# Optimization experiments

Hardware: AMD Instinct MI355X
Metric: run time of the kernel (lower is better)

Reference implementation:

```python
import jax, jax.numpy as jnp
import numpy as np
import math

E = 500_000   # edges
N = 2_000     # nodes (small so duplicate (src,dst) pairs form real groups)
D = 128       # embedding_dim == n_heads*qkv_dim
H = 8         # heads
DK = 16       # qkv_dim
HH = 256      # hyper hidden
EMBD = 2      # hyper embd_dim
CLIP = 10.0   # tanh_clipping


def setup_inputs() -> dict:
    key = jax.random.key(0)
    ks = jax.random.split(key, 12)
    # shared_nodes: inverse indices of unique edge (src,dst) columns (reset() preprocessing)
    rng = np.random.default_rng(0)
    edge_indices = rng.integers(0, N, size=(2, E))
    _, inv = np.unique(edge_indices, axis=1, return_inverse=True)
    shared_nodes = jnp.asarray(inv.reshape(-1), dtype=jnp.int32)

    def lin(k, shape, fan_in):
        return jax.random.normal(k, shape, jnp.float32) / np.sqrt(fan_in)

    return {
        "pref": jax.random.uniform(ks[0], (2,), jnp.float32),
        "dists": jax.random.uniform(ks[1], (E, 2), jnp.float32),
        "edge_emb": jax.random.normal(ks[2], (E, D), jnp.float32),
        "shared_nodes": shared_nodes,
        "fc1_w": lin(ks[3], (HH, 2), 2), "fc1_b": jnp.zeros((HH,), jnp.float32),
        "fc2_w": lin(ks[4], (HH, HH), HH), "fc2_b": jnp.zeros((HH,), jnp.float32),
        "fc3_w": lin(ks[5], (2 * EMBD, HH), HH), "fc3_b": jnp.zeros((2 * EMBD,), jnp.float32),
        "wq_w": lin(ks[6], (D * H * DK, EMBD), EMBD),
        "wk_w": lin(ks[7], (D * H * DK, EMBD), EMBD),
    }


def reference(pref, dists, edge_emb, shared_nodes,
              fc1_w, fc1_b, fc2_w, fc2_b, fc3_w, fc3_b, wq_w, wk_w):
    # --- assign(pref): hypernetwork producing Wq, Wk (no activations, per source) ---
    h = pref @ fc1_w.T + fc1_b
    h = h @ fc2_w.T + fc2_b
    mid = h @ fc3_w.T + fc3_b                    # [4]
    Wq = (mid[:EMBD] @ wq_w.T).reshape(D, H * DK)
    Wk = (mid[EMBD:2 * EMBD] @ wk_w.T).reshape(D, H * DK)

    # --- reset(): scalarized distances + group means over shared edge groups ---
    d = pref[0] * dists[:, 0] + pref[1] * dists[:, 1]   # [E]
    n_edges = edge_emb.shape[0]
    seg = shared_nodes
    group_sums = jax.ops.segment_sum(edge_emb, seg, num_segments=n_edges)
    counts = jax.ops.segment_sum(jnp.ones((n_edges,), edge_emb.dtype), seg,
                                 num_segments=n_edges)
    group_means = group_sums / jnp.clip(counts, 1.0)[:, None]
    q = group_means[seg]                          # [E, D]

    # --- forward(): edge-wise multi-head dot score, tanh clip, group softmax ---
    fq = (q @ Wq.T).reshape(n_edges, H, DK)       # F.linear(q, Wq) (D == H*DK)
    fk = (edge_emb @ Wk.T).reshape(n_edges, H, DK)
    score = (fq * fk).sum(-1).mean(-1) / math.sqrt(D) - d / math.sqrt(2.0)
    score = CLIP * jnp.tanh(score)

    seg_max = jax.ops.segment_max(score, seg, num_segments=n_edges)
    ex = jnp.exp(score - seg_max[seg])
    denom = jax.ops.segment_sum(ex, seg, num_segments=n_edges)
    probs = ex / denom[seg]
    return probs[:, None]                         # [E, 1]
```

## Files before the change

kernel.cpp:

```cpp
#include <hip/hip_runtime.h>
#include <math.h>

#define DD 128
#define HHID 256
#define SLOTS 8


__global__ void k_setup(const float* __restrict__ pref,
                        const float* __restrict__ fc1_w, const float* __restrict__ fc1_b,
                        const float* __restrict__ fc2_w, const float* __restrict__ fc2_b,
                        const float* __restrict__ fc3_w, const float* __restrict__ fc3_b,
                        const float* __restrict__ wq_w, const float* __restrict__ wk_w,
                        const int* __restrict__ seg, unsigned* __restrict__ cs,
                        int* __restrict__ mem, float* __restrict__ M_, int E_) {
    if (blockIdx.x >= 64) {
        int base = ((int)(blockIdx.x - 64) * blockDim.x + threadIdx.x) * 4;
        if (base + 3 < E_) {
            int4 s4 = *(const int4*)&seg[base];
            unsigned j0 = atomicAdd(&cs[s4.x], 1u);
            unsigned j1 = atomicAdd(&cs[s4.y], 1u);
            unsigned j2 = atomicAdd(&cs[s4.z], 1u);
            unsigned j3 = atomicAdd(&cs[s4.w], 1u);
            if (j0 < SLOTS) mem[(size_t)s4.x * SLOTS + j0] = base + 0;
            if (j1 < SLOTS) mem[(size_t)s4.y * SLOTS + j1] = base + 1;
            if (j2 < SLOTS) mem[(size_t)s4.z * SLOTS + j2] = base + 2;
            if (j3 < SLOTS) mem[(size_t)s4.w * SLOTS + j3] = base + 3;
        } else {
            for (int e = base; e < E_; ++e) {
                int g = seg[e];
                unsigned j = atomicAdd(&cs[g], 1u);
                if (j < SLOTS) mem[(size_t)g * SLOTS + j] = e;
            }
        }
        return;
    }
    __shared__ float h1[HHID];
    __shared__ float h2[HHID];
    __shared__ float mid[4];
    __shared__ float wqv[2 * DD];
    int t = threadIdx.x;
    float p0 = pref[0], p1 = pref[1];
    h1[t] = fc1_w[t * 2 + 0] * p0 + fc1_w[t * 2 + 1] * p1 + fc1_b[t];
    __syncthreads();
    float acc = fc2_b[t];
    for (int i = 0; i < HHID; ++i) acc += fc2_w[t * HHID + i] * h1[i];
    h2[t] = acc;
    __syncthreads();
    if (t < 4) {
        float m = fc3_b[t];
        for (int i = 0; i < HHID; ++i) m += fc3_w[t * HHID + i] * h2[i];
        mid[t] = m;
    }
    __syncthreads();
    float m0 = mid[0], m1 = mid[1], m2 = mid[2], m3 = mid[3];
    {
        int a = t & 127, rh = t >> 7;
        int r = blockIdx.x * 2 + rh;
        wqv[rh * DD + a] = wq_w[(a * DD + r) * 2 + 0] * m0 + wq_w[(a * DD + r) * 2 + 1] * m1;
    }
    __syncthreads();
    int rh = t >> 7;
    int r = blockIdx.x * 2 + rh;
    int c = t & 127;
    const float scale = 0.011048543456f;
    float s = 0.f;
    for (int a = 0; a < DD; ++a) {
        float wk = wk_w[(a * DD + c) * 2 + 0] * m2 + wk_w[(a * DD + c) * 2 + 1] * m3;
        s += wqv[rh * DD + a] * wk;
    }
    M_[r * DD + c] = s * scale;
}

__global__ void k_glist(const unsigned* __restrict__ cs, int* __restrict__ glist,
                        int* __restrict__ nctr, int E_) {
    __shared__ int lcnt;
    __shared__ int lbase;
    int t = threadIdx.x;
    if (t == 0) lcnt = 0;
    __syncthreads();
    int base = (blockIdx.x * blockDim.x + t) * 4;
    bool c0 = false, c1 = false, c2 = false, c3 = false;
    if (base + 3 < E_) {
        uint4 c4 = *(const uint4*)&cs[base];
        c0 = c4.x >= 2u; c1 = c4.y >= 2u; c2 = c4.z >= 2u; c3 = c4.w >= 2u;
    } else {
        if (base + 0 < E_) c0 = cs[base + 0] >= 2u;
        if (base + 1 < E_) c1 = cs[base + 1] >= 2u;
        if (base + 2 < E_) c2 = cs[base + 2] >= 2u;
        if (base + 3 < E_) c3 = cs[base + 3] >= 2u;
    }
    int m = (int)c0 + (int)c1 + (int)c2 + (int)c3;
    int lpos = 0;
    if (m) lpos = atomicAdd(&lcnt, m);
    __syncthreads();
    if (t == 0 && lcnt) lbase = atomicAdd(&nctr[1], lcnt);
    __syncthreads();
    if (m) {
        int p = lbase + lpos;
        if (c0) glist[p++] = base + 0;
        if (c1) glist[p++] = base + 1;
        if (c2) glist[p++] = base + 2;
        if (c3) glist[p++] = base + 3;
    }
}

__global__ __launch_bounds__(256) void k_fused(const int* __restrict__ glist,
                                               const int* __restrict__ nctr,
                                               const unsigned* __restrict__ cs,
                                               const int* __restrict__ mem,
                                               const float4* __restrict__ M4,
                                               const float4* __restrict__ emb4,
                                               const float2* __restrict__ emb2,
                                               const float2* __restrict__ dists2,
                                               const float* __restrict__ pref,
                                               float* __restrict__ out) {
    __shared__ float meanT[DD * 32];
    __shared__ float gtile[32 * DD];
    int t = threadIdx.x;
    int ng = nctr[1];
    int ntile = (ng + 31) >> 5;
    float p0 = pref[0], p1 = pref[1];
    for (int tile = blockIdx.x; tile < ntile; tile += gridDim.x) {
        int i0 = tile * 32;
        {
            int gi = t & 31;
            int kq = t >> 5;
            int i = i0 + gi;
            float4 s0 = make_float4(0.f, 0.f, 0.f, 0.f), s1 = s0, s2 = s0, s3 = s0;
            float inv = 0.f;
            if (i < ng) {
                int g = glist[i];
                unsigned c = cs[g];
                int cm = (int)(c < (unsigned)SLOTS ? c : (unsigned)SLOTS);
                inv = 1.0f / (float)c;
                for (int j = 0; j < cm; ++j) {
                    int e = mem[(size_t)g * SLOTS + j];
                    float4 v0 = emb4[(size_t)e * 32 + kq + 0];
                    float4 v1 = emb4[(size_t)e * 32 + kq + 8];
                    float4 v2 = emb4[(size_t)e * 32 + kq + 16];
                    float4 v3 = emb4[(size_t)e * 32 + kq + 24];
                    s0.x += v0.x; s0.y += v0.y; s0.z += v0.z; s0.w += v0.w;
                    s1.x += v1.x; s1.y += v1.y; s1.z += v1.z; s1.w += v1.w;
                    s2.x += v2.x; s2.y += v2.y; s2.z += v2.z; s2.w += v2.w;
                    s3.x += v3.x; s3.y += v3.y; s3.z += v3.z; s3.w += v3.w;
                }
            }
            int k0 = (kq + 0) * 4, k1 = (kq + 8) * 4, k2 = (kq + 16) * 4, k3 = (kq + 24) * 4;
            meanT[(k0 + 0) * 32 + gi] = s0.x * inv; meanT[(k0 + 1) * 32 + gi] = s0.y * inv;
            meanT[(k0 + 2) * 32 + gi] = s0.z * inv; meanT[(k0 + 3) * 32 + gi] = s0.w * inv;
            meanT[(k1 + 0) * 32 + gi] = s1.x * inv; meanT[(k1 + 1) * 32 + gi] = s1.y * inv;
            meanT[(k1 + 2) * 32 + gi] = s1.z * inv; meanT[(k1 + 3) * 32 + gi] = s1.w * inv;
            meanT[(k2 + 0) * 32 + gi] = s2.x * inv; meanT[(k2 + 1) * 32 + gi] = s2.y * inv;
            meanT[(k2 + 2) * 32 + gi] = s2.z * inv; meanT[(k2 + 3) * 32 + gi] = s2.w * inv;
            meanT[(k3 + 0) * 32 + gi] = s3.x * inv; meanT[(k3 + 1) * 32 + gi] = s3.y * inv;
            meanT[(k3 + 2) * 32 + gi] = s3.z * inv; meanT[(k3 + 3) * 32 + gi] = s3.w * inv;
        }
        __syncthreads();
        {
            int cseg = t & 31;
            int g4 = (t >> 5) * 4;
            float4 acc0 = make_float4(0.f, 0.f, 0.f, 0.f);
            float4 acc1 = acc0, acc2 = acc0, acc3 = acc0;
            #pragma unroll 4
            for (int k = 0; k < DD; ++k) {
                float4 mv = *(const float4*)&meanT[k * 32 + g4];
                float4 Mr = M4[k * 32 + cseg];
                acc0.x += mv.x * Mr.x; acc0.y += mv.x * Mr.y; acc0.z += mv.x * Mr.z; acc0.w += mv.x * Mr.w;
                acc1.x += mv.y * Mr.x; acc1.y += mv.y * Mr.y; acc1.z += mv.y * Mr.z; acc1.w += mv.y * Mr.w;
                acc2.x += mv.z * Mr.x; acc2.y += mv.z * Mr.y; acc2.z += mv.z * Mr.z; acc2.w += mv.z * Mr.w;
                acc3.x += mv.w * Mr.x; acc3.y += mv.w * Mr.y; acc3.z += mv.w * Mr.z; acc3.w += mv.w * Mr.w;
            }
            *(float4*)&gtile[(g4 + 0) * DD + cseg * 4] = acc0;
            *(float4*)&gtile[(g4 + 1) * DD + cseg * 4] = acc1;
            *(float4*)&gtile[(g4 + 2) * DD + cseg * 4] = acc2;
            *(float4*)&gtile[(g4 + 3) * DD + cseg * 4] = acc3;
        }
        __syncthreads();
        {
            int w = t >> 6;
            int lane = t & 63;
            for (int q = 0; q < 8; ++q) {
                int gl = w * 8 + q;
                int i = i0 + gl;
                if (i >= ng) continue;
                int g = glist[i];
                unsigned c = cs[g];
                int cm = (int)(c < (unsigned)SLOTS ? c : (unsigned)SLOTS);
                int e_lane = (lane < cm) ? mem[(size_t)g * SLOTS + lane] : 0;
                float2 tv = *(const float2*)&gtile[gl * DD + 2 * lane];
                float s_mine = 0.f;
                for (int j = 0; j < cm; ++j) {
                    int e = __shfl(e_lane, j, 64);
                    float2 kv = emb2[(size_t)e * 64 + lane];
                    float d = tv.x * kv.x + tv.y * kv.y;
                    for (int off = 32; off; off >>= 1) d += __shfl_xor(d, off, 64);
                    if (lane == j) s_mine = d;
                }
                if (lane < cm) {
                    float2 dd = dists2[e_lane];
                    float de = p0 * dd.x + p1 * dd.y;
                    s_mine = 10.0f * tanhf(s_mine - de * 0.7071067811865475f);
                }
                float v = (lane < cm) ? s_mine : -3.0e38f;
                for (int off = 32; off; off >>= 1) v = fmaxf(v, __shfl_xor(v, off, 64));
                float ex = (lane < cm) ? __expf(s_mine - v) : 0.f;
                float sm = ex;
                for (int off = 32; off; off >>= 1) sm += __shfl_xor(sm, off, 64);
                if (lane < cm) out[e_lane] = ex / sm;
            }
        }
        __syncthreads();
    }
}

extern "C" void kernel_launch(void* const* d_in, const int* in_sizes, int n_in,
                              void* d_out, int out_size, void* d_ws, size_t ws_size,
                              hipStream_t stream) {
    const float* pref  = (const float*)d_in[0];
    const float* dists = (const float*)d_in[1];
    const float* emb   = (const float*)d_in[2];
    const int*   seg   = (const int*)d_in[3];
    const float* fc1_w = (const float*)d_in[4];
    const float* fc1_b = (const float*)d_in[5];
    const float* fc2_w = (const float*)d_in[6];
    const float* fc2_b = (const float*)d_in[7];
    const float* fc3_w = (const float*)d_in[8];
    const float* fc3_b = (const float*)d_in[9];
    const float* wq_w  = (const float*)d_in[10];
    const float* wk_w  = (const float*)d_in[11];
    int E_ = in_sizes[3];
    float* out = (float*)d_out;

    char* ws = (char*)d_ws;
    int*      nctr = (int*)ws;
    unsigned* cs   = (unsigned*)(ws + 256);
    size_t zero_bytes = 256 + (size_t)E_ * 4;
    char* p = ws + ((zero_bytes + 255) & ~(size_t)255);
    int*   glist = (int*)p;   p += ((size_t)E_ * 4 + 255) & ~(size_t)255;
    float* M_    = (float*)p; p += (size_t)DD * DD * 4;
    int*   mem   = (int*)p;   p += (size_t)E_ * SLOTS * 4;
    if ((size_t)(p - ws) > ws_size) return;

    hipMemsetAsync(ws, 0, zero_bytes, stream);
    hipMemsetD32Async((hipDeviceptr_t)out, 0x3f800000u, (size_t)E_, stream);

    int tb = 256;
    int eb4 = (E_ + tb * 4 - 1) / (tb * 4);
    k_setup<<<64 + eb4, tb, 0, stream>>>(pref, fc1_w, fc1_b, fc2_w, fc2_b, fc3_w, fc3_b,
                                         wq_w, wk_w, seg, cs, mem, M_, E_);
    k_glist<<<eb4, tb, 0, stream>>>(cs, glist, nctr, E_);
    k_fused<<<1024, 256, 0, stream>>>(glist, nctr, cs, mem, (const float4*)M_,
                                      (const float4*)emb, (const float2*)emb,
                                      (const float2*)dists, pref, out);
}
```

Before: 418.5 us.

## Fold group-list compaction into fused kernel and output init into setup

Removes the separate k_glist kernel. Each fused block now scans its own contiguous range of group ids and builds a local list of multi-edge groups in shared memory, capped at LMAX entries. The output fill of ones moves from a memset into k_setup, and the extra counter memset is dropped. Together these cut two launches and a global atomic compaction pass. In exchange there is possible load imbalance across blocks and a silent correctness risk if more than 512 multi-edge groups fall in one block's range.

```diff
diff --git a/kernel.cpp b/kernel.cpp
--- a/kernel.cpp
+++ b/kernel.cpp
@@ -4,6 +4,8 @@
 #define DD 128
 #define HHID 256
 #define SLOTS 8
+#define NBF 1024
+#define LMAX 512
 
 
 __global__ void k_setup(const float* __restrict__ pref,
@@ -12,11 +14,13 @@
                         const float* __restrict__ fc3_w, const float* __restrict__ fc3_b,
                         const float* __restrict__ wq_w, const float* __restrict__ wk_w,
                         const int* __restrict__ seg, unsigned* __restrict__ cs,
-                        int* __restrict__ mem, float* __restrict__ M_, int E_) {
+                        int* __restrict__ mem, float* __restrict__ out,
+                        float* __restrict__ M_, int E_) {
     if (blockIdx.x >= 64) {
         int base = ((int)(blockIdx.x - 64) * blockDim.x + threadIdx.x) * 4;
         if (base + 3 < E_) {
             int4 s4 = *(const int4*)&seg[base];
+            *(float4*)&out[base] = make_float4(1.f, 1.f, 1.f, 1.f);
             unsigned j0 = atomicAdd(&cs[s4.x], 1u);
             unsigned j1 = atomicAdd(&cs[s4.y], 1u);
             unsigned j2 = atomicAdd(&cs[s4.z], 1u);
@@ -27,6 +31,7 @@
             if (j3 < SLOTS) mem[(size_t)s4.w * SLOTS + j3] = base + 3;
         } else {
             for (int e = base; e < E_; ++e) {
+                out[e] = 1.0f;
                 int g = seg[e];
                 unsigned j = atomicAdd(&cs[g], 1u);
                 if (j < SLOTS) mem[(size_t)g * SLOTS + j] = e;
@@ -71,65 +76,43 @@
     M_[r * DD + c] = s * scale;
 }
 
-__global__ void k_glist(const unsigned* __restrict__ cs, int* __restrict__ glist,
-                        int* __restrict__ nctr, int E_) {
-    __shared__ int lcnt;
-    __shared__ int lbase;
-    int t = threadIdx.x;
-    if (t == 0) lcnt = 0;
-    __syncthreads();
-    int base = (blockIdx.x * blockDim.x + t) * 4;
-    bool c0 = false, c1 = false, c2 = false, c3 = false;
-    if (base + 3 < E_) {
-        uint4 c4 = *(const uint4*)&cs[base];
-        c0 = c4.x >= 2u; c1 = c4.y >= 2u; c2 = c4.z >= 2u; c3 = c4.w >= 2u;
-    } else {
-        if (base + 0 < E_) c0 = cs[base + 0] >= 2u;
-        if (base + 1 < E_) c1 = cs[base + 1] >= 2u;
-        if (base + 2 < E_) c2 = cs[base + 2] >= 2u;
-        if (base + 3 < E_) c3 = cs[base + 3] >= 2u;
-    }
-    int m = (int)c0 + (int)c1 + (int)c2 + (int)c3;
-    int lpos = 0;
-    if (m) lpos = atomicAdd(&lcnt, m);
-    __syncthreads();
-    if (t == 0 && lcnt) lbase = atomicAdd(&nctr[1], lcnt);
-    __syncthreads();
-    if (m) {
-        int p = lbase + lpos;
-        if (c0) glist[p++] = base + 0;
-        if (c1) glist[p++] = base + 1;
-        if (c2) glist[p++] = base + 2;
-        if (c3) glist[p++] = base + 3;
-    }
-}
-
-__global__ __launch_bounds__(256) void k_fused(const int* __restrict__ glist,
-                                               const int* __restrict__ nctr,
-                                               const unsigned* __restrict__ cs,
+__global__ __launch_bounds__(256) void k_fused(const unsigned* __restrict__ cs,
                                                const int* __restrict__ mem,
                                                const float4* __restrict__ M4,
                                                const float4* __restrict__ emb4,
                                                const float2* __restrict__ emb2,
                                                const float2* __restrict__ dists2,
                                                const float* __restrict__ pref,
-                                               float* __restrict__ out) {
+                                               float* __restrict__ out, int E_) {
     __shared__ float meanT[DD * 32];
     __shared__ float gtile[32 * DD];
+    __shared__ int glist_l[LMAX];
+    __shared__ int lcnt;
     int t = threadIdx.x;
-    int ng = nctr[1];
-    int ntile = (ng + 31) >> 5;
+    int C = (E_ + (int)gridDim.x - 1) / (int)gridDim.x;
+    int g0 = (int)blockIdx.x * C;
+    if (g0 >= E_) return;
+    int cnt = min(C, E_ - g0);
+    if (t == 0) lcnt = 0;
+    __syncthreads();
+    for (int i = t; i < cnt; i += 256) {
+        if (cs[g0 + i] >= 2u) {
+            int p = atomicAdd(&lcnt, 1);
+            if (p < LMAX) glist_l[p] = g0 + i;
+        }
+    }
+    __syncthreads();
+    int nl = min(lcnt, LMAX);
     float p0 = pref[0], p1 = pref[1];
-    for (int tile = blockIdx.x; tile < ntile; tile += gridDim.x) {
-        int i0 = tile * 32;
+    for (int i0 = 0; i0 < nl; i0 += 32) {
+        int act = min(nl - i0, 32);
         {
             int gi = t & 31;
             int kq = t >> 5;
-            int i = i0 + gi;
             float4 s0 = make_float4(0.f, 0.f, 0.f, 0.f), s1 = s0, s2 = s0, s3 = s0;
             float inv = 0.f;
-            if (i < ng) {
-                int g = glist[i];
+            if (gi < act) {
+                int g = glist_l[i0 + gi];
                 unsigned c = cs[g];
                 int cm = (int)(c < (unsigned)SLOTS ? c : (unsigned)SLOTS);
                 inv = 1.0f / (float)c;
@@ -146,34 +129,37 @@
                 }
             }
             int k0 = (kq + 0) * 4, k1 = (kq + 8) * 4, k2 = (kq + 16) * 4, k3 = (kq + 24) * 4;
-            meanT[(k0 + 0) * 32 + gi] = s0.x * inv; meanT[(k0 + 1) * 32 + gi] = s0.y * inv;
-            meanT[(k0 + 2) * 32 + gi] = s0.z * inv; meanT[(k0 + 3) * 32 + gi] = s0.w * inv;
-            meanT[(k1 + 0) * 32 + gi] = s1.x * inv; meanT[(k1 + 1) * 32 + gi] = s1.y * inv;
-            meanT[(k1 + 2) * 32 + gi] = s1.z * inv; meanT[(k1 + 3) * 32 + gi] = s1.w * inv;
-            meanT[(k2 + 0) * 32 + gi] = s2.x * inv; meanT[(k2 + 1) * 32 + gi] = s2.y * inv;
-            meanT[(k2 + 2) * 32 + gi] = s2.z * inv; meanT[(k2 + 3) * 32 + gi] = s2.w * inv;
-            meanT[(k3 + 0) * 32 + gi] = s3.x * inv; meanT[(k3 + 1) * 32 + gi] = s3.y * inv;
-            meanT[(k3 + 2) * 32 + gi] = s3.z * inv; meanT[(k3 + 3) * 32 + gi] = s3.w * inv;
+            int gi2 = gi;
+            meanT[(k0 + 0) * 32 + gi2] = s0.x * inv; meanT[(k0 + 1) * 32 + gi2] = s0.y * inv;
+            meanT[(k0 + 2) * 32 + gi2] = s0.z * inv; meanT[(k0 + 3) * 32 + gi2] = s0.w * inv;
+            meanT[(k1 + 0) * 32 + gi2] = s1.x * inv; meanT[(k1 + 1) * 32 + gi2] = s1.y * inv;
+            meanT[(k1 + 2) * 32 + gi2] = s1.z * inv; meanT[(k1 + 3) * 32 + gi2] = s1.w * inv;
+            meanT[(k2 + 0) * 32 + gi2] = s2.x * inv; meanT[(k2 + 1) * 32 + gi2] = s2.y * inv;
+            meanT[(k2 + 2) * 32 + gi2] = s2.z * inv; meanT[(k2 + 3) * 32 + gi2] = s2.w * inv;
+            meanT[(k3 + 0) * 32 + gi2] = s3.x * inv; meanT[(k3 + 1) * 32 + gi2] = s3.y * inv;
+            meanT[(k3 + 2) * 32 + gi2] = s3.z * inv; meanT[(k3 + 3) * 32 + gi2] = s3.w * inv;
         }
         __syncthreads();
         {
             int cseg = t & 31;
             int g4 = (t >> 5) * 4;
-            float4 acc0 = make_float4(0.f, 0.f, 0.f, 0.f);
-            float4 acc1 = acc0, acc2 = acc0, acc3 = acc0;
-            #pragma unroll 4
-            for (int k = 0; k < DD; ++k) {
-                float4 mv = *(const float4*)&meanT[k * 32 + g4];
-                float4 Mr = M4[k * 32 + cseg];
-                acc0.x += mv.x * Mr.x; acc0.y += mv.x * Mr.y; acc0.z += mv.x * Mr.z; acc0.w += mv.x * Mr.w;
-                acc1.x += mv.y * Mr.x; acc1.y += mv.y * Mr.y; acc1.z += mv.y * Mr.z; acc1.w += mv.y * Mr.w;
-                acc2.x += mv.z * Mr.x; acc2.y += mv.z * Mr.y; acc2.z += mv.z * Mr.z; acc2.w += mv.z * Mr.w;
-                acc3.x += mv.w * Mr.x; acc3.y += mv.w * Mr.y; acc3.z += mv.w * Mr.z; acc3.w += mv.w * Mr.w;
-            }
-            *(float4*)&gtile[(g4 + 0) * DD + cseg * 4] = acc0;
-            *(float4*)&gtile[(g4 + 1) * DD + cseg * 4] = acc1;
-            *(float4*)&gtile[(g4 + 2) * DD + cseg * 4] = acc2;
-            *(float4*)&gtile[(g4 + 3) * DD + cseg * 4] = acc3;
+            if (g4 < act) {
+                float4 acc0 = make_float4(0.f, 0.f, 0.f, 0.f);
+                float4 acc1 = acc0, acc2 = acc0, acc3 = acc0;
+                #pragma unroll 4
+                for (int k = 0; k < DD; ++k) {
+                    float4 mv = *(const float4*)&meanT[k * 32 + g4];
+                    float4 Mr = M4[k * 32 + cseg];
+                    acc0.x += mv.x * Mr.x; acc0.y += mv.x * Mr.y; acc0.z += mv.x * Mr.z; acc0.w += mv.x * Mr.w;
+                    acc1.x += mv.y * Mr.x; acc1.y += mv.y * Mr.y; acc1.z += mv.y * Mr.z; acc1.w += mv.y * Mr.w;
+                    acc2.x += mv.z * Mr.x; acc2.y += mv.z * Mr.y; acc2.z += mv.z * Mr.z; acc2.w += mv.z * Mr.w;
+                    acc3.x += mv.w * Mr.x; acc3.y += mv.w * Mr.y; acc3.z += mv.w * Mr.z; acc3.w += mv.w * Mr.w;
+                }
+                *(float4*)&gtile[(g4 + 0) * DD + cseg * 4] = acc0;
+                *(float4*)&gtile[(g4 + 1) * DD + cseg * 4] = acc1;
+                *(float4*)&gtile[(g4 + 2) * DD + cseg * 4] = acc2;
+                *(float4*)&gtile[(g4 + 3) * DD + cseg * 4] = acc3;
+            }
         }
         __syncthreads();
         {
@@ -181,9 +167,8 @@
             int lane = t & 63;
             for (int q = 0; q < 8; ++q) {
                 int gl = w * 8 + q;
-                int i = i0 + gl;
-                if (i >= ng) continue;
-                int g = glist[i];
+                if (gl >= act) continue;
+                int g = glist_l[i0 + gl];
                 unsigned c = cs[g];
                 int cm = (int)(c < (unsigned)SLOTS ? c : (unsigned)SLOTS);
                 int e_lane = (lane < cm) ? mem[(size_t)g * SLOTS + lane] : 0;
@@ -232,24 +217,19 @@
     float* out = (float*)d_out;
 
     char* ws = (char*)d_ws;
-    int*      nctr = (int*)ws;
-    unsigned* cs   = (unsigned*)(ws + 256);
-    size_t zero_bytes = 256 + (size_t)E_ * 4;
-    char* p = ws + ((zero_bytes + 255) & ~(size_t)255);
-    int*   glist = (int*)p;   p += ((size_t)E_ * 4 + 255) & ~(size_t)255;
-    float* M_    = (float*)p; p += (size_t)DD * DD * 4;
-    int*   mem   = (int*)p;   p += (size_t)E_ * SLOTS * 4;
+    unsigned* cs = (unsigned*)ws;
+    char* p = ws + (((size_t)E_ * 4 + 255) & ~(size_t)255);
+    float* M_  = (float*)p; p += (size_t)DD * DD * 4;
+    int*   mem = (int*)p;   p += (size_t)E_ * SLOTS * 4;
     if ((size_t)(p - ws) > ws_size) return;
 
-    hipMemsetAsync(ws, 0, zero_bytes, stream);
-    hipMemsetD32Async((hipDeviceptr_t)out, 0x3f800000u, (size_t)E_, stream);
+    hipMemsetAsync(ws, 0, (size_t)E_ * 4, stream);
 
     int tb = 256;
     int eb4 = (E_ + tb * 4 - 1) / (tb * 4);
     k_setup<<<64 + eb4, tb, 0, stream>>>(pref, fc1_w, fc1_b, fc2_w, fc2_b, fc3_w, fc3_b,
-                                         wq_w, wk_w, seg, cs, mem, M_, E_);
-    k_glist<<<eb4, tb, 0, stream>>>(cs, glist, nctr, E_);
-    k_fused<<<1024, 256, 0, stream>>>(glist, nctr, cs, mem, (const float4*)M_,
-                                      (const float4*)emb, (const float2*)emb,
-                                      (const float2*)dists, pref, out);
+                                         wq_w, wk_w, seg, cs, mem, out, M_, E_);
+    k_fused<<<NBF, 256, 0, stream>>>(cs, mem, (const float4*)M_,
+                                     (const float4*)emb, (const float2*)emb,
+                                     (const float2*)dists, pref, out, E_);
 }
```

After: 428.1 us. 1.02x slower.

## Fuse group-list construction and output init into setup scatter kernel

Applied to the files above, without the earlier changes.

The group list of multi-edge segments is now built in the scatter pass: the thread whose atomic returns slot index 1 appends that group id, which removes the separate k_glist kernel and its full pass over the counts array. The output buffer is filled with ones in the same pass, replacing a separate memset launch. The fused kernel also skips the matmul for empty tail rows of the last tile. Group order in the list becomes nondeterministic, which does not affect correctness.

```diff
diff --git a/kernel.cpp b/kernel.cpp
--- a/kernel.cpp
+++ b/kernel.cpp
@@ -12,11 +12,21 @@
                         const float* __restrict__ fc3_w, const float* __restrict__ fc3_b,
                         const float* __restrict__ wq_w, const float* __restrict__ wk_w,
                         const int* __restrict__ seg, unsigned* __restrict__ cs,
-                        int* __restrict__ mem, float* __restrict__ M_, int E_) {
+                        int* __restrict__ mem, int* __restrict__ glist,
+                        int* __restrict__ nctr, float* __restrict__ out,
+                        float* __restrict__ M_, int E_) {
     if (blockIdx.x >= 64) {
-        int base = ((int)(blockIdx.x - 64) * blockDim.x + threadIdx.x) * 4;
+        __shared__ int lcnt;
+        __shared__ int lbase;
+        int t = threadIdx.x;
+        if (t == 0) lcnt = 0;
+        __syncthreads();
+        int base = ((int)(blockIdx.x - 64) * blockDim.x + t) * 4;
+        int ids[4];
+        int nap = 0;
         if (base + 3 < E_) {
             int4 s4 = *(const int4*)&seg[base];
+            *(float4*)&out[base] = make_float4(1.f, 1.f, 1.f, 1.f);
             unsigned j0 = atomicAdd(&cs[s4.x], 1u);
             unsigned j1 = atomicAdd(&cs[s4.y], 1u);
             unsigned j2 = atomicAdd(&cs[s4.z], 1u);
@@ -25,12 +35,27 @@
             if (j1 < SLOTS) mem[(size_t)s4.y * SLOTS + j1] = base + 1;
             if (j2 < SLOTS) mem[(size_t)s4.z * SLOTS + j2] = base + 2;
             if (j3 < SLOTS) mem[(size_t)s4.w * SLOTS + j3] = base + 3;
+            if (j0 == 1u) ids[nap++] = s4.x;
+            if (j1 == 1u) ids[nap++] = s4.y;
+            if (j2 == 1u) ids[nap++] = s4.z;
+            if (j3 == 1u) ids[nap++] = s4.w;
         } else {
             for (int e = base; e < E_; ++e) {
+                out[e] = 1.0f;
                 int g = seg[e];
                 unsigned j = atomicAdd(&cs[g], 1u);
                 if (j < SLOTS) mem[(size_t)g * SLOTS + j] = e;
-            }
+                if (j == 1u) ids[nap++] = g;
+            }
+        }
+        int lpos = 0;
+        if (nap) lpos = atomicAdd(&lcnt, nap);
+        __syncthreads();
+        if (t == 0 && lcnt) lbase = atomicAdd(&nctr[0], lcnt);
+        __syncthreads();
+        if (nap) {
+            int p = lbase + lpos;
+            for (int k = 0; k < nap; ++k) glist[p + k] = ids[k];
         }
         return;
     }
@@ -69,39 +94,6 @@
         s += wqv[rh * DD + a] * wk;
     }
     M_[r * DD + c] = s * scale;
-}
-
-__global__ void k_glist(const unsigned* __restrict__ cs, int* __restrict__ glist,
-                        int* __restrict__ nctr, int E_) {
-    __shared__ int lcnt;
-    __shared__ int lbase;
-    int t = threadIdx.x;
-    if (t == 0) lcnt = 0;
-    __syncthreads();
-    int base = (blockIdx.x * blockDim.x + t) * 4;
-    bool c0 = false, c1 = false, c2 = false, c3 = false;
-    if (base + 3 < E_) {
-        uint4 c4 = *(const uint4*)&cs[base];
-        c0 = c4.x >= 2u; c1 = c4.y >= 2u; c2 = c4.z >= 2u; c3 = c4.w >= 2u;
-    } else {
-        if (base + 0 < E_) c0 = cs[base + 0] >= 2u;
-        if (base + 1 < E_) c1 = cs[base + 1] >= 2u;
-        if (base + 2 < E_) c2 = cs[base + 2] >= 2u;
-        if (base + 3 < E_) c3 = cs[base + 3] >= 2u;
-    }
-    int m = (int)c0 + (int)c1 + (int)c2 + (int)c3;
-    int lpos = 0;
-    if (m) lpos = atomicAdd(&lcnt, m);
-    __syncthreads();
-    if (t == 0 && lcnt) lbase = atomicAdd(&nctr[1], lcnt);
-    __syncthreads();
-    if (m) {
-        int p = lbase + lpos;
-        if (c0) glist[p++] = base + 0;
-        if (c1) glist[p++] = base + 1;
-        if (c2) glist[p++] = base + 2;
-        if (c3) glist[p++] = base + 3;
-    }
 }
 
 __global__ __launch_bounds__(256) void k_fused(const int* __restrict__ glist,
@@ -117,19 +109,19 @@
     __shared__ float meanT[DD * 32];
     __shared__ float gtile[32 * DD];
     int t = threadIdx.x;
-    int ng = nctr[1];
+    int ng = nctr[0];
     int ntile = (ng + 31) >> 5;
     float p0 = pref[0], p1 = pref[1];
     for (int tile = blockIdx.x; tile < ntile; tile += gridDim.x) {
         int i0 = tile * 32;
+        int act = min(ng - i0, 32);
         {
             int gi = t & 31;
             int kq = t >> 5;
-            int i = i0 + gi;
             float4 s0 = make_float4(0.f, 0.f, 0.f, 0.f), s1 = s0, s2 = s0, s3 = s0;
             float inv = 0.f;
-            if (i < ng) {
-                int g = glist[i];
+            if (gi < act) {
+                int g = glist[i0 + gi];
                 unsigned c = cs[g];
                 int cm = (int)(c < (unsigned)SLOTS ? c : (unsigned)SLOTS);
                 inv = 1.0f / (float)c;
@@ -159,21 +151,23 @@
         {
             int cseg = t & 31;
             int g4 = (t >> 5) * 4;
-            float4 acc0 = make_float4(0.f, 0.f, 0.f, 0.f);
-            float4 acc1 = acc0, acc2 = acc0, acc3 = acc0;
-            #pragma unroll 4
-            for (int k = 0; k < DD; ++k) {
-                float4 mv = *(const float4*)&meanT[k * 32 + g4];
-                float4 Mr = M4[k * 32 + cseg];
-                acc0.x += mv.x * Mr.x; acc0.y += mv.x * Mr.y; acc0.z += mv.x * Mr.z; acc0.w += mv.x * Mr.w;
-                acc1.x += mv.y * Mr.x; acc1.y += mv.y * Mr.y; acc1.z += mv.y * Mr.z; acc1.w += mv.y * Mr.w;
-                acc2.x += mv.z * Mr.x; acc2.y += mv.z * Mr.y; acc2.z += mv.z * Mr.z; acc2.w += mv.z * Mr.w;
-                acc3.x += mv.w * Mr.x; acc3.y += mv.w * Mr.y; acc3.z += mv.w * Mr.z; acc3.w += mv.w * Mr.w;
-            }
-            *(float4*)&gtile[(g4 + 0) * DD + cseg * 4] = acc0;
-            *(float4*)&gtile[(g4 + 1) * DD + cseg * 4] = acc1;
-            *(float4*)&gtile[(g4 + 2) * DD + cseg * 4] = acc2;
-            *(float4*)&gtile[(g4 + 3) * DD + cseg * 4] = acc3;
+            if (g4 < act) {
+                float4 acc0 = make_float4(0.f, 0.f, 0.f, 0.f);
+                float4 acc1 = acc0, acc2 = acc0, acc3 = acc0;
+                #pragma unroll 4
+                for (int k = 0; k < DD; ++k) {
+                    float4 mv = *(const float4*)&meanT[k * 32 + g4];
+                    float4 Mr = M4[k * 32 + cseg];
+                    acc0.x += mv.x * Mr.x; acc0.y += mv.x * Mr.y; acc0.z += mv.x * Mr.z; acc0.w += mv.x * Mr.w;
+                    acc1.x += mv.y * Mr.x; acc1.y += mv.y * Mr.y; acc1.z += mv.y * Mr.z; acc1.w += mv.y * Mr.w;
+                    acc2.x += mv.z * Mr.x; acc2.y += mv.z * Mr.y; acc2.z += mv.z * Mr.z; acc2.w += mv.z * Mr.w;
+                    acc3.x += mv.w * Mr.x; acc3.y += mv.w * Mr.y; acc3.z += mv.w * Mr.z; acc3.w += mv.w * Mr.w;
+                }
+                *(float4*)&gtile[(g4 + 0) * DD + cseg * 4] = acc0;
+                *(float4*)&gtile[(g4 + 1) * DD + cseg * 4] = acc1;
+                *(float4*)&gtile[(g4 + 2) * DD + cseg * 4] = acc2;
+                *(float4*)&gtile[(g4 + 3) * DD + cseg * 4] = acc3;
+            }
         }
         __syncthreads();
         {
@@ -181,9 +175,8 @@
             int lane = t & 63;
             for (int q = 0; q < 8; ++q) {
                 int gl = w * 8 + q;
-                int i = i0 + gl;
-                if (i >= ng) continue;
-                int g = glist[i];
+                if (gl >= act) continue;
+                int g = glist[i0 + gl];
                 unsigned c = cs[g];
                 int cm = (int)(c < (unsigned)SLOTS ? c : (unsigned)SLOTS);
                 int e_lane = (lane < cm) ? mem[(size_t)g * SLOTS + lane] : 0;
@@ -242,13 +235,11 @@
     if ((size_t)(p - ws) > ws_size) return;
 
     hipMemsetAsync(ws, 0, zero_bytes, stream);
-    hipMemsetD32Async((hipDeviceptr_t)out, 0x3f800000u, (size_t)E_, stream);
 
     int tb = 256;
     int eb4 = (E_ + tb * 4 - 1) / (tb * 4);
     k_setup<<<64 + eb4, tb, 0, stream>>>(pref, fc1_w, fc1_b, fc2_w, fc2_b, fc3_w, fc3_b,
-                                         wq_w, wk_w, seg, cs, mem, M_, E_);
-    k_glist<<<eb4, tb, 0, stream>>>(cs, glist, nctr, E_);
+                                         wq_w, wk_w, seg, cs, mem, glist, nctr, out, M_, E_);
     k_fused<<<1024, 256, 0, stream>>>(glist, nctr, cs, mem, (const float4*)M_,
                                       (const float4*)emb, (const float2*)emb,
                                       (const float2*)dists, pref, out);
```

Measured after the change: 409.8 us. -2.1%, faster.
